# Performance work log

Hardware: AMD Instinct MI355X
Metric: run time of the kernel (lower is better)

The kernel has to match this reference:

```python
import jax, jax.numpy as jnp
import numpy as np

B, E, S, D = 32, 64, 50, 300   # batch, sentences/essay, words/sentence, word dim
F = 100                        # conv filters (cnn_lstm_convunits_size)
H = 100                        # lstm units (cnn_lstm_att_pool_size)
W_WIN = 5                      # word window length


def setup_inputs() -> dict:
    key = jax.random.key(0)
    ks = jax.random.split(key, 12)
    n = lambda k, shape: (jax.random.normal(k, shape, jnp.float32) * 0.05)
    return {
        "essays": jax.random.normal(ks[0], (B, E, S, D), jnp.float32),
        "conv_k": n(ks[1], (1, W_WIN, D, F)),      # HWIO
        "conv_b": jnp.zeros((F,), jnp.float32),
        "att1_mat": n(ks[2], (F, F)),
        "att1_bias": n(ks[3], (F,)),
        "att1_vec": n(ks[4], (F, 1)),
        "lstm_W": n(ks[5], (F + H, 4 * H)),        # TF BasicLSTMCell kernel, gate order i,j,f,o
        "lstm_b": jnp.zeros((4 * H,), jnp.float32),
        "att2_mat": n(ks[6], (H, H)),
        "att2_bias": n(ks[7], (H,)),
        "att2_vec": n(ks[8], (H, 1)),
        "dense_w": n(ks[9], (H, 1)),
        "dense_b": jnp.zeros((1,), jnp.float32),
    }


def reference(essays, conv_k, conv_b, att1_mat, att1_bias, att1_vec,
              lstm_W, lstm_b, att2_mat, att2_bias, att2_vec,
              dense_w, dense_b):
    # conv2d, kernel [1, w_window_len], SAME padding, relu  -> [B,E,S,F]
    conv1 = jax.lax.conv_general_dilated(
        essays, conv_k, window_strides=(1, 1), padding="SAME",
        dimension_numbers=("NHWC", "HWIO", "NHWC"))
    conv1 = jax.nn.relu(conv1 + conv_b)

    # attention pooling over words (axis=2)
    a1 = jnp.tanh(jnp.einsum("besf,fg->besg", conv1, att1_mat) + att1_bias)
    a1 = jnp.einsum("besg,go->beso", a1, att1_vec)          # [B,E,S,1]
    a1 = jax.nn.softmax(a1, axis=2)
    sent = jnp.sum(a1 * conv1, axis=2)                       # [B,E,F]

    # BasicLSTMCell (forget_bias=1.0, gate order i,j,f,o) over sentence axis
    hdim = lstm_b.shape[0] // 4
    bsz = essays.shape[0]

    def step(carry, xt):
        c, h = carry
        z = jnp.concatenate([xt, h], axis=1) @ lstm_W + lstm_b
        i, j, f, o = jnp.split(z, 4, axis=1)
        c = c * jax.nn.sigmoid(f + 1.0) + jax.nn.sigmoid(i) * jnp.tanh(j)
        h = jax.nn.sigmoid(o) * jnp.tanh(c)
        return (c, h), h

    init = (jnp.zeros((bsz, hdim), sent.dtype), jnp.zeros((bsz, hdim), sent.dtype))
    xs = jnp.swapaxes(sent, 0, 1)                            # [E,B,F]
    _, hs = jax.lax.scan(step, init, xs)
    lstm = jnp.swapaxes(hs, 0, 1)                            # [B,E,H]

    # attention pooling over sentences (axis=1)
    a2 = jnp.tanh(jnp.einsum("beh,hg->beg", lstm, att2_mat) + att2_bias)
    a2 = jnp.einsum("beg,go->beo", a2, att2_vec)             # [B,E,1]
    a2 = jax.nn.softmax(a2, axis=1)
    essay_repr = jnp.sum(a2 * lstm, axis=1)                  # [B,H]

    preds = jax.nn.sigmoid(essay_repr @ dense_w + dense_b).reshape(-1)  # [B]
    return preds
```

## Files before the change

kernel.cpp:

```cpp
#include <hip/hip_runtime.h>
#include <hip/hip_bf16.h>
#include <stdint.h>

#define Bsz 32
#define Esz 64
#define Ssz 50
#define Dsz 300
#define Fsz 100
#define Hsz 100
#define WWIN 5

#define PX   328
#define PC   136
#define KT_CONV 50
#define NTILES  7
#define MTILES  4
#define NGRP 2214

typedef __attribute__((ext_vector_type(8))) short bf16x8;
typedef __attribute__((ext_vector_type(8))) unsigned short u16x8;
typedef __attribute__((ext_vector_type(4))) float f32x4;

__device__ __forceinline__ float sigmoid_fast(float x) {
    return 1.0f / (1.0f + __expf(-x));
}
__device__ __forceinline__ float tanhf_fast(float x) {
    const float ax = fabsf(x);
    const float e = __expf(2.0f * ax);
    const float t = 1.0f - 2.0f / (e + 1.0f);
    return copysignf(t, x);
}

__device__ __forceinline__ unsigned short f2bf(float x) {
    union { __hip_bfloat16 h; unsigned short u; } cv;
    cv.h = __float2bfloat16(x);
    return cv.u;
}
__device__ __forceinline__ unsigned int f2bf2(float lo, float hi) {
    union { __hip_bfloat162 h2; unsigned int u; } cv;
    cv.h2 = __float22bfloat162_rn(make_float2(lo, hi));
    return cv.u;
}
__device__ __forceinline__ float bf2f(unsigned short b) {
    union { uint32_t u; float f; } v; v.u = ((uint32_t)b) << 16;
    return v.f;
}

#define N_BTGC (KT_CONV * 112 * 32)
#define N_BTGA (4 * 112 * 32)
#define N_BTGW (4 * 400 * 32)

__global__ __launch_bounds__(256) void prep_kernel(
    const float* __restrict__ conv_k, const float* __restrict__ att1_mat,
    const float* __restrict__ lstm_W,
    unsigned short* __restrict__ BtgC, unsigned short* __restrict__ BtgA,
    unsigned short* __restrict__ BtgW)
{
    const int total = N_BTGC + N_BTGA + N_BTGW;
    for (int i = blockIdx.x * 256 + threadIdx.x; i < total; i += gridDim.x * 256) {
        if (i < N_BTGC) {
            const int kt = i / (112 * 32);
            const int r  = i % (112 * 32);
            const int n  = r / 32;
            const int kk = r % 32;
            const int w  = kt / 10;
            const int d  = (kt % 10) * 32 + kk;
            float val = (d < Dsz && n < Fsz) ? conv_k[((size_t)w * Dsz + d) * Fsz + n] : 0.f;
            BtgC[i] = f2bf(val);
        } else if (i < N_BTGC + N_BTGA) {
            const int j  = i - N_BTGC;
            const int kt = j / (112 * 32);
            const int r  = j % (112 * 32);
            const int n  = r / 32;
            const int kk = r % 32;
            const int k  = kt * 32 + kk;
            float val = (k < Fsz && n < Fsz) ? att1_mat[(size_t)k * Fsz + n] : 0.f;
            BtgA[j] = f2bf(val);
        } else {
            const int j  = i - N_BTGC - N_BTGA;
            const int kt = j / (400 * 32);
            const int r  = j % (400 * 32);
            const int n  = r / 32;
            const int kk = r % 32;
            const int k  = kt * 32 + kk;
            float val = (k < Fsz) ? lstm_W[(size_t)k * 400 + n] : 0.f;
            BtgW[j] = f2bf(val);
        }
    }
}

template<int G>
__device__ __forceinline__ void conv_loadB(
    const unsigned short* __restrict__ BtgC, int boff0, int boff1, bool has1,
    bf16x8 (&bR)[5][2])
{
#pragma unroll
    for (int i = 0; i < 5; ++i) {
        const int kt = G * 5 + i;
        bR[i][0] = *reinterpret_cast<const bf16x8*>(BtgC + kt * 3584 + boff0);
        bR[i][1] = has1 ? *reinterpret_cast<const bf16x8*>(BtgC + kt * 3584 + boff1)
                        : (bf16x8)0;
    }
}

template<int G>
__device__ __forceinline__ void conv_compute(
    const unsigned short* buf0, const unsigned short* buf1,
    const int (&abase)[MTILES], bool has1,
    const bf16x8 (&bR)[5][2], f32x4 (&acc)[2][MTILES][2])
{
#pragma unroll
    for (int i = 0; i < 5; ++i) {
        const int kt  = G * 5 + i;
        const int w   = kt / 10;
        const int t   = kt % 10;
        const int off = w * PX + t * 32;
#pragma unroll
        for (int mt = 0; mt < MTILES; ++mt) {
            const bf16x8 af0 = *reinterpret_cast<const bf16x8*>(&buf0[abase[mt] + off]);
            const bf16x8 af1 = *reinterpret_cast<const bf16x8*>(&buf1[abase[mt] + off]);
            acc[0][mt][0] = __builtin_amdgcn_mfma_f32_16x16x32_bf16(af0, bR[i][0], acc[0][mt][0], 0, 0, 0);
            acc[1][mt][0] = __builtin_amdgcn_mfma_f32_16x16x32_bf16(af1, bR[i][0], acc[1][mt][0], 0, 0, 0);
            if (has1) {
                acc[0][mt][1] = __builtin_amdgcn_mfma_f32_16x16x32_bf16(af0, bR[i][1], acc[0][mt][1], 0, 0, 0);
                acc[1][mt][1] = __builtin_amdgcn_mfma_f32_16x16x32_bf16(af1, bR[i][1], acc[1][mt][1], 0, 0, 0);
            }
        }
    }
}

__global__ __launch_bounds__(256, 2) void conv_att1_kernel(
    const float* __restrict__ essays,
    const unsigned short* __restrict__ BtgC,
    const unsigned short* __restrict__ BtgA,
    const float* __restrict__ conv_b,
    const float* __restrict__ att1_bias,
    const float* __restrict__ att1_vec,
    unsigned short* __restrict__ sent_bf)
{
    __shared__ __align__(16) unsigned short buf[2][54 * PX];
    __shared__ float u_s[2][64];
    __shared__ float alpha_s[2][64];

    const int be0 = blockIdx.x * 2;
    const int tid = threadIdx.x;
    const int lane = tid & 63;
    const int wid  = tid >> 6;
    const int ln   = lane & 15;
    const int qd   = lane >> 4;

    if (tid < 128) u_s[tid >> 6][tid & 63] = 0.f;

#pragma unroll
    for (int es = 0; es < 2; ++es) {
        const float* in_g = essays + (size_t)(be0 + es) * (Ssz * Dsz);
        float4 va[9], vb[9];
        int rr[9], cc[9];
        bool hv[9], fv[9], gv[9];
#pragma unroll
        for (int it = 0; it < 9; ++it) {
            const int g  = tid + it * 256;
            const int r  = g / 41;
            const int c8 = (g - r * 41) * 8;
            const int s  = r - 2;
            gv[it] = (g < NGRP);
            hv[it] = gv[it] && (s >= 0) && (s < Ssz) && (c8 < Dsz);
            fv[it] = hv[it] && (c8 + 8 <= Dsz);
            const float* base = in_g + (hv[it] ? (s * Dsz + c8) : 0);
            va[it] = *reinterpret_cast<const float4*>(base);
            vb[it] = *reinterpret_cast<const float4*>(fv[it] ? base + 4 : base);
            rr[it] = r; cc[it] = c8;
        }
#pragma unroll
        for (int it = 0; it < 9; ++it) {
            if (!gv[it]) continue;
            const float e0 = hv[it] ? va[it].x : 0.f;
            const float e1 = hv[it] ? va[it].y : 0.f;
            const float e2 = hv[it] ? va[it].z : 0.f;
            const float e3 = hv[it] ? va[it].w : 0.f;
            const float e4 = fv[it] ? vb[it].x : 0.f;
            const float e5 = fv[it] ? vb[it].y : 0.f;
            const float e6 = fv[it] ? vb[it].z : 0.f;
            const float e7 = fv[it] ? vb[it].w : 0.f;
            uint4 o;
            o.x = f2bf2(e0, e1);
            o.y = f2bf2(e2, e3);
            o.z = f2bf2(e4, e5);
            o.w = f2bf2(e6, e7);
            *reinterpret_cast<uint4*>(&buf[es][rr[it] * PX + cc[it]]) = o;
        }
    }
    __syncthreads();

    const int nt0 = wid;
    const int nt1 = wid + 4;
    const bool has1 = (nt1 < NTILES);
    const int boff0 = (nt0 * 16 + ln) * 32 + 8 * qd;
    const int boff1 = (nt1 * 16 + ln) * 32 + 8 * qd;

    int abase[MTILES];
#pragma unroll
    for (int mt = 0; mt < MTILES; ++mt) {
        const int m = mt * 16 + ln;
        abase[mt] = (m < Ssz ? m : Ssz - 1) * PX + 8 * qd;
    }

    f32x4 acc[2][MTILES][2];
#pragma unroll
    for (int es = 0; es < 2; ++es)
#pragma unroll
        for (int mt = 0; mt < MTILES; ++mt) { acc[es][mt][0] = (f32x4)0.f; acc[es][mt][1] = (f32x4)0.f; }

    {
        const unsigned short* b0p = buf[0];
        const unsigned short* b1p = buf[1];
        bf16x8 bX[5][2], bY[5][2];
        conv_loadB<0>(BtgC, boff0, boff1, has1, bX);
        conv_loadB<1>(BtgC, boff0, boff1, has1, bY);
        conv_compute<0>(b0p, b1p, abase, has1, bX, acc);
        conv_loadB<2>(BtgC, boff0, boff1, has1, bX);
        conv_compute<1>(b0p, b1p, abase, has1, bY, acc);
        conv_loadB<3>(BtgC, boff0, boff1, has1, bY);
        conv_compute<2>(b0p, b1p, abase, has1, bX, acc);
        conv_loadB<4>(BtgC, boff0, boff1, has1, bX);
        conv_compute<3>(b0p, b1p, abase, has1, bY, acc);
        conv_loadB<5>(BtgC, boff0, boff1, has1, bY);
        conv_compute<4>(b0p, b1p, abase, has1, bX, acc);
        conv_loadB<6>(BtgC, boff0, boff1, has1, bX);
        conv_compute<5>(b0p, b1p, abase, has1, bY, acc);
        conv_loadB<7>(BtgC, boff0, boff1, has1, bY);
        conv_compute<6>(b0p, b1p, abase, has1, bX, acc);
        conv_loadB<8>(BtgC, boff0, boff1, has1, bX);
        conv_compute<7>(b0p, b1p, abase, has1, bY, acc);
        conv_loadB<9>(BtgC, boff0, boff1, has1, bY);
        conv_compute<8>(b0p, b1p, abase, has1, bX, acc);
        conv_compute<9>(b0p, b1p, abase, has1, bY, acc);
    }

    bf16x8 a1b[4][2];
#pragma unroll
    for (int kt = 0; kt < 4; ++kt) {
        a1b[kt][0] = *reinterpret_cast<const bf16x8*>(BtgA + kt * 3584 + boff0);
        a1b[kt][1] = has1 ? *reinterpret_cast<const bf16x8*>(BtgA + kt * 3584 + boff1)
                          : (bf16x8)0;
    }
    __syncthreads();

    {
        const float bias0 = conv_b[nt0 * 16 + ln];
        const int n_g1 = nt1 * 16 + ln;
        const bool g1ok = has1 && (n_g1 < Fsz);
        const float bias1 = g1ok ? conv_b[n_g1] : 0.f;
#pragma unroll
        for (int es = 0; es < 2; ++es) {
#pragma unroll
            for (int mt = 0; mt < MTILES; ++mt) {
#pragma unroll
                for (int j = 0; j < 4; ++j) {
                    const int m_row = mt * 16 + qd * 4 + j;
                    buf[es][m_row * PC + nt0 * 16 + ln] = f2bf(fmaxf(acc[es][mt][0][j] + bias0, 0.f));
                    if (g1ok)
                        buf[es][m_row * PC + n_g1] = f2bf(fmaxf(acc[es][mt][1][j] + bias1, 0.f));
                }
            }
        }
    }
    for (int idx = tid; idx < 2 * 64 * 2; idx += 256) {
        const int es = idx >> 7;
        const int r2 = idx & 127;
        const int row = r2 >> 1;
        const int c = 112 + (r2 & 1) * 8;
        *reinterpret_cast<u16x8*>(&buf[es][row * PC + c]) = (u16x8)0;
    }
    __syncthreads();

    f32x4 acc2[2][MTILES][2];
#pragma unroll
    for (int es = 0; es < 2; ++es)
#pragma unroll
        for (int mt = 0; mt < MTILES; ++mt) { acc2[es][mt][0] = (f32x4)0.f; acc2[es][mt][1] = (f32x4)0.f; }

#pragma unroll
    for (int kt = 0; kt < 4; ++kt) {
#pragma unroll
        for (int es = 0; es < 2; ++es) {
#pragma unroll
            for (int mt = 0; mt < MTILES; ++mt) {
                const bf16x8 af = *reinterpret_cast<const bf16x8*>(
                    &buf[es][(mt * 16 + ln) * PC + kt * 32 + 8 * qd]);
                acc2[es][mt][0] = __builtin_amdgcn_mfma_f32_16x16x32_bf16(af, a1b[kt][0], acc2[es][mt][0], 0, 0, 0);
                if (has1)
                    acc2[es][mt][1] = __builtin_amdgcn_mfma_f32_16x16x32_bf16(af, a1b[kt][1], acc2[es][mt][1], 0, 0, 0);
            }
        }
    }

    {
        const int g0 = nt0 * 16 + ln;
        const float b1v0 = att1_bias[g0];
        const float vv0  = att1_vec[g0];
        const int g1 = nt1 * 16 + ln;
        const bool g1v = has1 && (g1 < Fsz);
        const float b1v1 = g1v ? att1_bias[g1] : 0.f;
        const float vv1  = g1v ? att1_vec[g1]  : 0.f;
#pragma unroll
        for (int es = 0; es < 2; ++es) {
#pragma unroll
            for (int mt = 0; mt < MTILES; ++mt) {
#pragma unroll
                for (int j = 0; j < 4; ++j) {
                    const int m_row = mt * 16 + qd * 4 + j;
                    float val = 0.f;
                    if (m_row < Ssz) {
                        val = tanhf_fast(acc2[es][mt][0][j] + b1v0) * vv0;
                        if (g1v) val += tanhf_fast(acc2[es][mt][1][j] + b1v1) * vv1;
                    }
                    val += __shfl_xor(val, 1);
                    val += __shfl_xor(val, 2);
                    val += __shfl_xor(val, 4);
                    val += __shfl_xor(val, 8);
                    if (ln == 0 && m_row < Ssz) atomicAdd(&u_s[es][m_row], val);
                }
            }
        }
    }
    __syncthreads();

    if (wid < 2) {
        const float uv = (lane < Ssz) ? u_s[wid][lane] : -1e30f;
        float m = uv;
#pragma unroll
        for (int off = 32; off > 0; off >>= 1) m = fmaxf(m, __shfl_xor(m, off));
        float e = (lane < Ssz) ? __expf(uv - m) : 0.f;
        float sum = e;
#pragma unroll
        for (int off = 32; off > 0; off >>= 1) sum += __shfl_xor(sum, off);
        alpha_s[wid][lane] = e / sum;
    }
    __syncthreads();

    {
        const int es = tid >> 7;
        const int f  = tid & 127;
        unsigned short v = 0;
        if (f < Fsz) {
            float a = 0.f;
            for (int s = 0; s < Ssz; ++s) a += alpha_s[es][s] * bf2f(buf[es][s * PC + f]);
            v = f2bf(a);
        }
        sent_bf[(size_t)(be0 + es) * 128 + f] = v;
    }
}

__global__ __launch_bounds__(256) void xpart_kernel(
    const unsigned short* __restrict__ sent_bf,
    const unsigned short* __restrict__ BtgW,
    const float* __restrict__ lstm_b,
    float* __restrict__ xpart)
{
    const int wid  = threadIdx.x >> 6;
    const int mt   = blockIdx.x * 4 + wid;
    const int lane = threadIdx.x & 63;
    const int ln   = lane & 15;
    const int qd   = lane >> 4;
    const int m0   = mt * 16;

    f32x4 acc[25];
#pragma unroll
    for (int nt = 0; nt < 25; ++nt) acc[nt] = (f32x4)0.f;

#pragma unroll
    for (int kt = 0; kt < 4; ++kt) {
        const bf16x8 a = *reinterpret_cast<const bf16x8*>(
            sent_bf + (size_t)(m0 + ln) * 128 + kt * 32 + 8 * qd);
#pragma unroll
        for (int nt = 0; nt < 25; ++nt) {
            const bf16x8 b = *reinterpret_cast<const bf16x8*>(
                BtgW + ((size_t)kt * 400 + nt * 16 + ln) * 32 + 8 * qd);
            acc[nt] = __builtin_amdgcn_mfma_f32_16x16x32_bf16(a, b, acc[nt], 0, 0, 0);
        }
    }

#pragma unroll
    for (int nt = 0; nt < 25; ++nt) {
        const int col = nt * 16 + ln;
        const float bias = lstm_b[col];
#pragma unroll
        for (int j = 0; j < 4; ++j) {
            const int row = m0 + qd * 4 + j;
            xpart[(size_t)row * 400 + col] = acc[nt][j] + bias;
        }
    }
}

__global__ __launch_bounds__(448) void lstm_att2_kernel(
    const float* __restrict__ xpart,
    const float* __restrict__ lstm_W,
    const float* __restrict__ att2_mat,
    const float* __restrict__ att2_bias,
    const float* __restrict__ att2_vec,
    const float* __restrict__ dense_w,
    const float* __restrict__ dense_b,
    float* __restrict__ out)
{
    __shared__ __align__(16) float h_s[Hsz];
    __shared__ float z_s[400];
    __shared__ __align__(16) float hist[Esz][Hsz];
    __shared__ float w2_s[Esz * Hsz];
    __shared__ float u2_s[Esz];
    __shared__ float alpha2_s[Esz];
    __shared__ float repr_s[Hsz];

    const int b = blockIdx.x;
    const int tid = threadIdx.x;
    const bool actv = tid < 400;

    float w[100];
    if (actv) {
#pragma unroll
        for (int k = 0; k < 100; ++k) w[k] = lstm_W[(size_t)(Fsz + k) * 400 + tid];
    }
    float c = 0.f;
    if (tid < Hsz) h_s[tid] = 0.f;
    __syncthreads();

    float xp_cur = actv ? xpart[(size_t)b * Esz * 400 + tid] : 0.f;
    const float4* h4 = reinterpret_cast<const float4*>(h_s);

    for (int t = 0; t < Esz; ++t) {
        const float xp_next = (actv && (t + 1) < Esz)
            ? xpart[((size_t)b * Esz + t + 1) * 400 + tid] : 0.f;
        if (actv) {
            float z0 = xp_cur, z1 = 0.f, z2 = 0.f, z3 = 0.f;
#pragma unroll
            for (int k4 = 0; k4 < 25; ++k4) {
                const float4 hv = h4[k4];
                z0 += hv.x * w[4 * k4 + 0];
                z1 += hv.y * w[4 * k4 + 1];
                z2 += hv.z * w[4 * k4 + 2];
                z3 += hv.w * w[4 * k4 + 3];
            }
            z_s[tid] = (z0 + z1) + (z2 + z3);
        }
        __syncthreads();

        if (tid < Hsz) {
            const float zi = z_s[tid];
            const float zj = z_s[tid + 100];
            const float zf = z_s[tid + 200];
            const float zo = z_s[tid + 300];
            c = c * sigmoid_fast(zf + 1.0f) + sigmoid_fast(zi) * tanhf_fast(zj);
            const float h = sigmoid_fast(zo) * tanhf_fast(c);
            h_s[tid] = h;
            hist[t][tid] = h;
        }
        __syncthreads();
        xp_cur = xp_next;
    }

    for (int idx = tid; idx < Esz * Hsz; idx += 448) {
        const int e = idx / Hsz;
        const int g = idx - e * Hsz;
        const float* lp = hist[e];
        float a0 = 0.f, a1 = 0.f, a2 = 0.f, a3 = 0.f;
        for (int k = 0; k < Hsz; k += 4) {
            a0 += lp[k + 0] * att2_mat[(k + 0) * Hsz + g];
            a1 += lp[k + 1] * att2_mat[(k + 1) * Hsz + g];
            a2 += lp[k + 2] * att2_mat[(k + 2) * Hsz + g];
            a3 += lp[k + 3] * att2_mat[(k + 3) * Hsz + g];
        }
        w2_s[idx] = tanhf_fast(att2_bias[g] + ((a0 + a1) + (a2 + a3))) * att2_vec[g];
    }
    __syncthreads();

    if (tid < Esz) {
        float acc = 0.f;
        const float* wp = w2_s + tid * Hsz;
        for (int g = 0; g < Hsz; ++g) acc += wp[g];
        u2_s[tid] = acc;
    }
    __syncthreads();

    if (tid < 64) {
        const float uv = u2_s[tid];
        float m = uv;
#pragma unroll
        for (int off = 32; off > 0; off >>= 1) m = fmaxf(m, __shfl_xor(m, off));
        float e = __expf(uv - m);
        float sum = e;
#pragma unroll
        for (int off = 32; off > 0; off >>= 1) sum += __shfl_xor(sum, off);
        alpha2_s[tid] = e / sum;
    }
    __syncthreads();

    if (tid < Hsz) {
        float acc = 0.f;
        for (int e = 0; e < Esz; ++e) acc += alpha2_s[e] * hist[e][tid];
        repr_s[tid] = acc;
    }
    __syncthreads();

    if (tid == 0) {
        float acc = dense_b[0];
        for (int hh = 0; hh < Hsz; ++hh) acc += repr_s[hh] * dense_w[hh];
        out[b] = sigmoid_fast(acc);
    }
}

extern "C" void kernel_launch(void* const* d_in, const int* in_sizes, int n_in,
                              void* d_out, int out_size, void* d_ws, size_t ws_size,
                              hipStream_t stream) {
    const float* essays    = (const float*)d_in[0];
    const float* conv_k    = (const float*)d_in[1];
    const float* conv_b    = (const float*)d_in[2];
    const float* att1_mat  = (const float*)d_in[3];
    const float* att1_bias = (const float*)d_in[4];
    const float* att1_vec  = (const float*)d_in[5];
    const float* lstm_W    = (const float*)d_in[6];
    const float* lstm_b    = (const float*)d_in[7];
    const float* att2_mat  = (const float*)d_in[8];
    const float* att2_bias = (const float*)d_in[9];
    const float* att2_vec  = (const float*)d_in[10];
    const float* dense_w   = (const float*)d_in[11];
    const float* dense_b   = (const float*)d_in[12];

    float* out = (float*)d_out;

    char* ws = (char*)d_ws;
    unsigned short* sent_bf = (unsigned short*)ws;
    float* xpart = (float*)(ws + 524288);
    unsigned short* BtgC = (unsigned short*)(ws + 3801088);
    unsigned short* BtgA = (unsigned short*)(ws + 4159488);
    unsigned short* BtgW = (unsigned short*)(ws + 4188160);

    prep_kernel<<<512, 256, 0, stream>>>(conv_k, att1_mat, lstm_W, BtgC, BtgA, BtgW);
    conv_att1_kernel<<<Bsz * Esz / 2, 256, 0, stream>>>(
        essays, BtgC, BtgA, conv_b, att1_bias, att1_vec, sent_bf);
    xpart_kernel<<<32, 256, 0, stream>>>(sent_bf, BtgW, lstm_b, xpart);
    lstm_att2_kernel<<<Bsz, 448, 0, stream>>>(
        xpart, lstm_W, att2_mat, att2_bias, att2_vec, dense_w, dense_b, out);
}
```

Before: 208.9 us.

## Double-buffer LDS A-fragments and hoist weight loads ahead of staging

Restructures the conv and attention MFMA loops so the LDS A-fragments for the next k-step are loaded into an alternate register set while the current step's MFMAs run (register double-buffering). It also starts the first two global B-weight loads before the essay staging and raises wave priority around MFMA bursts with s_setprio. The goal is to hide LDS and global latency behind matrix work. The cost is higher register pressure at 2 waves/SIMD launch bounds, which could cause spills.

```diff
diff --git a/kernel.cpp b/kernel.cpp
--- a/kernel.cpp
+++ b/kernel.cpp
@@ -103,29 +103,78 @@
     }
 }
 
+template<int KT>
+__device__ __forceinline__ void conv_loadA(
+    const unsigned short* b0p, const unsigned short* b1p,
+    const int (&abase)[MTILES], bf16x8 (&a)[2][MTILES])
+{
+    constexpr int w   = KT / 10;
+    constexpr int t   = KT % 10;
+    constexpr int off = w * PX + t * 32;
+#pragma unroll
+    for (int mt = 0; mt < MTILES; ++mt) {
+        a[0][mt] = *reinterpret_cast<const bf16x8*>(&b0p[abase[mt] + off]);
+        a[1][mt] = *reinterpret_cast<const bf16x8*>(&b1p[abase[mt] + off]);
+    }
+}
+
+__device__ __forceinline__ void mfma16(
+    const bf16x8 (&a)[2][MTILES], const bf16x8 (&b)[2], bool has1,
+    f32x4 (&acc)[2][MTILES][2])
+{
+    __builtin_amdgcn_s_setprio(1);
+#pragma unroll
+    for (int es = 0; es < 2; ++es) {
+#pragma unroll
+        for (int mt = 0; mt < MTILES; ++mt) {
+            acc[es][mt][0] = __builtin_amdgcn_mfma_f32_16x16x32_bf16(a[es][mt], b[0], acc[es][mt][0], 0, 0, 0);
+            if (has1)
+                acc[es][mt][1] = __builtin_amdgcn_mfma_f32_16x16x32_bf16(a[es][mt], b[1], acc[es][mt][1], 0, 0, 0);
+        }
+    }
+    __builtin_amdgcn_s_setprio(0);
+}
+
+template<int KT>
+__device__ __forceinline__ void conv_kt(
+    const unsigned short* b0p, const unsigned short* b1p,
+    const int (&abase)[MTILES], bool has1, const bf16x8 (&b)[2],
+    bf16x8 (&aX)[2][MTILES], bf16x8 (&aY)[2][MTILES],
+    f32x4 (&acc)[2][MTILES][2])
+{
+    constexpr bool even = (KT % 2) == 0;
+    if constexpr (KT + 1 < KT_CONV) {
+        if constexpr (even) conv_loadA<KT + 1>(b0p, b1p, abase, aY);
+        else                conv_loadA<KT + 1>(b0p, b1p, abase, aX);
+    }
+    if constexpr (even) mfma16(aX, b, has1, acc);
+    else                mfma16(aY, b, has1, acc);
+}
+
 template<int G>
-__device__ __forceinline__ void conv_compute(
-    const unsigned short* buf0, const unsigned short* buf1,
-    const int (&abase)[MTILES], bool has1,
-    const bf16x8 (&bR)[5][2], f32x4 (&acc)[2][MTILES][2])
-{
-#pragma unroll
-    for (int i = 0; i < 5; ++i) {
-        const int kt  = G * 5 + i;
-        const int w   = kt / 10;
-        const int t   = kt % 10;
-        const int off = w * PX + t * 32;
-#pragma unroll
-        for (int mt = 0; mt < MTILES; ++mt) {
-            const bf16x8 af0 = *reinterpret_cast<const bf16x8*>(&buf0[abase[mt] + off]);
-            const bf16x8 af1 = *reinterpret_cast<const bf16x8*>(&buf1[abase[mt] + off]);
-            acc[0][mt][0] = __builtin_amdgcn_mfma_f32_16x16x32_bf16(af0, bR[i][0], acc[0][mt][0], 0, 0, 0);
-            acc[1][mt][0] = __builtin_amdgcn_mfma_f32_16x16x32_bf16(af1, bR[i][0], acc[1][mt][0], 0, 0, 0);
-            if (has1) {
-                acc[0][mt][1] = __builtin_amdgcn_mfma_f32_16x16x32_bf16(af0, bR[i][1], acc[0][mt][1], 0, 0, 0);
-                acc[1][mt][1] = __builtin_amdgcn_mfma_f32_16x16x32_bf16(af1, bR[i][1], acc[1][mt][1], 0, 0, 0);
-            }
-        }
+__device__ __forceinline__ void conv_group(
+    const unsigned short* b0p, const unsigned short* b1p,
+    const int (&abase)[MTILES], bool has1, const bf16x8 (&bR)[5][2],
+    bf16x8 (&aX)[2][MTILES], bf16x8 (&aY)[2][MTILES],
+    f32x4 (&acc)[2][MTILES][2])
+{
+    conv_kt<G * 5 + 0>(b0p, b1p, abase, has1, bR[0], aX, aY, acc);
+    conv_kt<G * 5 + 1>(b0p, b1p, abase, has1, bR[1], aX, aY, acc);
+    conv_kt<G * 5 + 2>(b0p, b1p, abase, has1, bR[2], aX, aY, acc);
+    conv_kt<G * 5 + 3>(b0p, b1p, abase, has1, bR[3], aX, aY, acc);
+    conv_kt<G * 5 + 4>(b0p, b1p, abase, has1, bR[4], aX, aY, acc);
+}
+
+template<int KT>
+__device__ __forceinline__ void att_loadA(
+    const unsigned short* b0p, const unsigned short* b1p,
+    const int (&abase2)[MTILES], bf16x8 (&a)[2][MTILES])
+{
+    constexpr int off = KT * 32;
+#pragma unroll
+    for (int mt = 0; mt < MTILES; ++mt) {
+        a[0][mt] = *reinterpret_cast<const bf16x8*>(&b0p[abase2[mt] + off]);
+        a[1][mt] = *reinterpret_cast<const bf16x8*>(&b1p[abase2[mt] + off]);
     }
 }
 
@@ -150,6 +199,23 @@
     const int qd   = lane >> 4;
 
     if (tid < 128) u_s[tid >> 6][tid & 63] = 0.f;
+
+    const int nt0 = wid;
+    const int nt1 = wid + 4;
+    const bool has1 = (nt1 < NTILES);
+    const int boff0 = (nt0 * 16 + ln) * 32 + 8 * qd;
+    const int boff1 = (nt1 * 16 + ln) * 32 + 8 * qd;
+
+    int abase[MTILES];
+#pragma unroll
+    for (int mt = 0; mt < MTILES; ++mt) {
+        const int m = mt * 16 + ln;
+        abase[mt] = (m < Ssz ? m : Ssz - 1) * PX + 8 * qd;
+    }
+
+    bf16x8 bX[5][2], bY[5][2];
+    conv_loadB<0>(BtgC, boff0, boff1, has1, bX);
+    conv_loadB<1>(BtgC, boff0, boff1, has1, bY);
 
 #pragma unroll
     for (int es = 0; es < 2; ++es) {
@@ -192,18 +258,8 @@
     }
     __syncthreads();
 
-    const int nt0 = wid;
-    const int nt1 = wid + 4;
-    const bool has1 = (nt1 < NTILES);
-    const int boff0 = (nt0 * 16 + ln) * 32 + 8 * qd;
-    const int boff1 = (nt1 * 16 + ln) * 32 + 8 * qd;
-
-    int abase[MTILES];
-#pragma unroll
-    for (int mt = 0; mt < MTILES; ++mt) {
-        const int m = mt * 16 + ln;
-        abase[mt] = (m < Ssz ? m : Ssz - 1) * PX + 8 * qd;
-    }
+    const unsigned short* b0p = buf[0];
+    const unsigned short* b1p = buf[1];
 
     f32x4 acc[2][MTILES][2];
 #pragma unroll
@@ -212,29 +268,26 @@
         for (int mt = 0; mt < MTILES; ++mt) { acc[es][mt][0] = (f32x4)0.f; acc[es][mt][1] = (f32x4)0.f; }
 
     {
-        const unsigned short* b0p = buf[0];
-        const unsigned short* b1p = buf[1];
-        bf16x8 bX[5][2], bY[5][2];
-        conv_loadB<0>(BtgC, boff0, boff1, has1, bX);
-        conv_loadB<1>(BtgC, boff0, boff1, has1, bY);
-        conv_compute<0>(b0p, b1p, abase, has1, bX, acc);
+        bf16x8 aX[2][MTILES], aY[2][MTILES];
+        conv_loadA<0>(b0p, b1p, abase, aX);
+        conv_group<0>(b0p, b1p, abase, has1, bX, aX, aY, acc);
         conv_loadB<2>(BtgC, boff0, boff1, has1, bX);
-        conv_compute<1>(b0p, b1p, abase, has1, bY, acc);
+        conv_group<1>(b0p, b1p, abase, has1, bY, aX, aY, acc);
         conv_loadB<3>(BtgC, boff0, boff1, has1, bY);
-        conv_compute<2>(b0p, b1p, abase, has1, bX, acc);
+        conv_group<2>(b0p, b1p, abase, has1, bX, aX, aY, acc);
         conv_loadB<4>(BtgC, boff0, boff1, has1, bX);
-        conv_compute<3>(b0p, b1p, abase, has1, bY, acc);
+        conv_group<3>(b0p, b1p, abase, has1, bY, aX, aY, acc);
         conv_loadB<5>(BtgC, boff0, boff1, has1, bY);
-        conv_compute<4>(b0p, b1p, abase, has1, bX, acc);
+        conv_group<4>(b0p, b1p, abase, has1, bX, aX, aY, acc);
         conv_loadB<6>(BtgC, boff0, boff1, has1, bX);
-        conv_compute<5>(b0p, b1p, abase, has1, bY, acc);
+        conv_group<5>(b0p, b1p, abase, has1, bY, aX, aY, acc);
         conv_loadB<7>(BtgC, boff0, boff1, has1, bY);
-        conv_compute<6>(b0p, b1p, abase, has1, bX, acc);
+        conv_group<6>(b0p, b1p, abase, has1, bX, aX, aY, acc);
         conv_loadB<8>(BtgC, boff0, boff1, has1, bX);
-        conv_compute<7>(b0p, b1p, abase, has1, bY, acc);
+        conv_group<7>(b0p, b1p, abase, has1, bY, aX, aY, acc);
         conv_loadB<9>(BtgC, boff0, boff1, has1, bY);
-        conv_compute<8>(b0p, b1p, abase, has1, bX, acc);
-        conv_compute<9>(b0p, b1p, abase, has1, bY, acc);
+        conv_group<8>(b0p, b1p, abase, has1, bX, aX, aY, acc);
+        conv_group<9>(b0p, b1p, abase, has1, bY, aX, aY, acc);
     }
 
     bf16x8 a1b[4][2];
@@ -280,19 +333,20 @@
 #pragma unroll
         for (int mt = 0; mt < MTILES; ++mt) { acc2[es][mt][0] = (f32x4)0.f; acc2[es][mt][1] = (f32x4)0.f; }
 
-#pragma unroll
-    for (int kt = 0; kt < 4; ++kt) {
-#pragma unroll
-        for (int es = 0; es < 2; ++es) {
-#pragma unroll
-            for (int mt = 0; mt < MTILES; ++mt) {
-                const bf16x8 af = *reinterpret_cast<const bf16x8*>(
-                    &buf[es][(mt * 16 + ln) * PC + kt * 32 + 8 * qd]);
-                acc2[es][mt][0] = __builtin_amdgcn_mfma_f32_16x16x32_bf16(af, a1b[kt][0], acc2[es][mt][0], 0, 0, 0);
-                if (has1)
-                    acc2[es][mt][1] = __builtin_amdgcn_mfma_f32_16x16x32_bf16(af, a1b[kt][1], acc2[es][mt][1], 0, 0, 0);
-            }
-        }
+    {
+        int abase2[MTILES];
+#pragma unroll
+        for (int mt = 0; mt < MTILES; ++mt) abase2[mt] = (mt * 16 + ln) * PC + 8 * qd;
+
+        bf16x8 aX[2][MTILES], aY[2][MTILES];
+        att_loadA<0>(b0p, b1p, abase2, aX);
+        att_loadA<1>(b0p, b1p, abase2, aY);
+        mfma16(aX, a1b[0], has1, acc2);
+        att_loadA<2>(b0p, b1p, abase2, aX);
+        mfma16(aY, a1b[1], has1, acc2);
+        att_loadA<3>(b0p, b1p, abase2, aY);
+        mfma16(aX, a1b[2], has1, acc2);
+        mfma16(aY, a1b[3], has1, acc2);
     }
 
     {
```

New measurement: 202.8 us. 3.0% less time.
